# Kernel tuning notes

Measured on AMD Instinct MI355X. Metric: run time of the kernel, lower is better.

## Reference

```python
import jax, jax.numpy as jnp
import numpy as np

EPS_ATTN = 1e-6
EPS_LN = 1e-5


def _layer_norm(x, g, b):
    m = jnp.mean(x, axis=-1, keepdims=True)
    v = jnp.mean((x - m) ** 2, axis=-1, keepdims=True)
    return (x - m) * jax.lax.rsqrt(v + EPS_LN) * g + b


def _linear_attention(q, k, v):
    # q,k,v: [N, L/S, H, D]; elu feature map (+1 keeps values positive)
    q = jax.nn.elu(q) + 1.0
    k = jax.nn.elu(k) + 1.0
    s_len = v.shape[1]
    v = v / s_len
    kv = jnp.einsum('nshd,nshv->nhdv', k, v)            # [N,H,D,D]
    z = 1.0 / (jnp.einsum('nlhd,nhd->nlh', q, k.sum(axis=1)) + EPS_ATTN)
    out = jnp.einsum('nlhd,nhdv->nlhv', q, kv) * z[..., None] * s_len
    return out


def setup_inputs() -> dict:
    key = jax.random.key(0)
    ks = jax.random.split(key, 8)
    N, L, S, H, D = 4, 4096, 4096, 8, 64
    sc = 0.05
    return {
        'x': jax.random.normal(ks[0], (N, L, H, D), jnp.float32),
        'source': jax.random.normal(ks[1], (N, S, H, D), jnp.float32),
        'wq': jax.random.normal(ks[2], (D, D), jnp.float32) * sc,
        'wk': jax.random.normal(ks[3], (D, D), jnp.float32) * sc,
        'wv': jax.random.normal(ks[4], (D, D), jnp.float32) * sc,
        'wmerge': jax.random.normal(ks[5], (D, D), jnp.float32) * sc,
        'w1': jax.random.normal(ks[6], (2 * D, 2 * D), jnp.float32) * sc,
        'w2': jax.random.normal(ks[7], (D, 2 * D), jnp.float32) * sc,
        'g1': jnp.ones((D,), jnp.float32),
        'b1': jnp.zeros((D,), jnp.float32),
        'g2': jnp.ones((D,), jnp.float32),
        'b2': jnp.zeros((D,), jnp.float32),
    }


def reference(x, source, wq, wk, wv, wmerge, w1, w2, g1, b1, g2, b2):
    # projections (torch Linear: y = x @ W.T), applied on last dim D=d_model
    q = jnp.einsum('nlhd,ed->nlhe', x, wq)
    k = jnp.einsum('nshd,ed->nshe', source, wk)
    v = jnp.einsum('nshd,ed->nshe', source, wv)
    message = _linear_attention(q, k, v)                # [N,L,H,D]
    message = jnp.einsum('nlhd,ed->nlhe', message, wmerge)
    message = _layer_norm(message, g1, b1)
    h = jnp.concatenate([x, message], axis=-1)          # [N,L,H,2D]
    h = jax.nn.relu(jnp.einsum('nlhd,ed->nlhe', h, w1))
    h = jnp.einsum('nlhd,ed->nlhe', h, w2)              # [N,L,H,D]
    h = _layer_norm(h, g2, b2)
    return x + h
```

## Files before the change

### kernel.cpp

```cpp
#include <hip/hip_runtime.h>
#include <cstdint>

#define NB 4
#define LL 4096
#define SS 4096
#define HH 8
#define DD 64
#define NHC (NB*HH)

typedef unsigned short ushort_t;
typedef __bf16 bf16x8 __attribute__((ext_vector_type(8)));
typedef float f32x4 __attribute__((ext_vector_type(4)));
typedef unsigned short u16x8 __attribute__((ext_vector_type(8)));
typedef unsigned short u16x4 __attribute__((ext_vector_type(4)));

__device__ __forceinline__ float bf2f(unsigned short u) {
    union { unsigned int i; float f; } v; v.i = ((unsigned int)u) << 16; return v.f;
}
__device__ __forceinline__ unsigned short f2bf(float f) {
    union { float ff; unsigned int i; } v; v.ff = f;
    unsigned int x = v.i;
    x += 0x7fffu + ((x >> 16) & 1u);
    return (unsigned short)(x >> 16);
}
__device__ __forceinline__ bool input_is_bf16(const void* g1) {
    return ((const unsigned short*)g1)[0] == 0x3F80u;
}

template<bool BF16>
__device__ __forceinline__ float ldgf(const void* p, size_t i) {
    if constexpr (BF16) return bf2f(((const unsigned short*)p)[i]);
    else                return ((const float*)p)[i];
}
template<bool BF16>
__device__ __forceinline__ u16x8 ld8(const void* p, size_t i) {
    if constexpr (BF16) {
        return *reinterpret_cast<const u16x8*>((const unsigned short*)p + i);
    } else {
        const float* f = (const float*)p + i;
        u16x8 o;
        #pragma unroll
        for (int j = 0; j < 8; ++j) o[j] = f2bf(f[j]);
        return o;
    }
}
__device__ __forceinline__ bf16x8 ldsA(const ushort_t* p) {
    return *reinterpret_cast<const bf16x8*>(p);
}
#define MFMA16(a,b,c) __builtin_amdgcn_mfma_f32_16x16x32_bf16(a,b,c,0,0,0)

template<bool BF16, int LC>
__device__ __forceinline__ void stage_w(const void* g, size_t goff, ushort_t* dst,
                                        int rows, int dstride, int tid) {
    int total8 = (rows << LC) >> 3;
    for (int i8 = tid; i8 < total8; i8 += 256) {
        int i = i8 << 3;
        int r = i >> LC, c = i & ((1 << LC) - 1);
        *reinterpret_cast<u16x8*>(dst + r * dstride + c) = ld8<BF16>(g, goff + i);
    }
}

__device__ __forceinline__ void red16(float v[4]) {
    #pragma unroll
    for (int m = 1; m < 16; m <<= 1) {
        #pragma unroll
        for (int r = 0; r < 4; ++r) v[r] += __shfl_xor(v[r], m);
    }
}

template<bool BF16>
__device__ void kv_body(const void* __restrict__ src, const void* __restrict__ wk,
                        const void* __restrict__ wv, float* __restrict__ kvg,
                        float* __restrict__ ksumg,
                        ushort_t* S, ushort_t* KT, ushort_t* VT)
{
    const int tid = threadIdx.x;
    const int lane = tid & 63, w = tid >> 6;
    const int lg = lane >> 4, l15 = lane & 15;
    const int bid = blockIdx.x;
    const int nh = bid >> 5, ch = bid & 31;
    const int n = nh >> 3, h = nh & 7;
    const int s0 = ch * 128;
    const f32x4 z4 = {0.f, 0.f, 0.f, 0.f};

    stage_w<BF16, 6>(wk, 0, KT, 64, 136, tid);
    stage_w<BF16, 6>(wv, 0, VT, 64, 136, tid);
    for (int i = tid; i < 128 * 8; i += 256) {
        int r = i >> 3, c8 = (i & 7) << 3;
        size_t gb = ((size_t)((size_t)n * SS + (s0 + r)) * HH + h) * DD + c8;
        *reinterpret_cast<u16x8*>(S + r * 72 + c8) = ld8<BF16>(src, gb);
    }
    __syncthreads();

    bf16x8 wkf[2][4], wvf[2][4];
    #pragma unroll
    for (int ks = 0; ks < 2; ++ks)
        #pragma unroll
        for (int nt = 0; nt < 4; ++nt) {
            wkf[ks][nt] = ldsA(KT + (nt * 16 + l15) * 136 + ks * 32 + lg * 8);
            wvf[ks][nt] = ldsA(VT + (nt * 16 + l15) * 136 + ks * 32 + lg * 8);
        }
    __syncthreads();

    float ksp[4] = {0.f, 0.f, 0.f, 0.f};
    #pragma unroll
    for (int mtt = 0; mtt < 2; ++mtt) {
        const int rowA = w * 32 + mtt * 16;
        bf16x8 af[2];
        #pragma unroll
        for (int ks = 0; ks < 2; ++ks)
            af[ks] = ldsA(S + (rowA + l15) * 72 + ks * 32 + lg * 8);
        f32x4 ka[4], va[4];
        #pragma unroll
        for (int nt = 0; nt < 4; ++nt) { ka[nt] = z4; va[nt] = z4; }
        #pragma unroll
        for (int ks = 0; ks < 2; ++ks)
            #pragma unroll
            for (int nt = 0; nt < 4; ++nt) {
                ka[nt] = MFMA16(af[ks], wkf[ks][nt], ka[nt]);
                va[nt] = MFMA16(af[ks], wvf[ks][nt], va[nt]);
            }
        #pragma unroll
        for (int nt = 0; nt < 4; ++nt) {
            u16x4 kp, vp;
            #pragma unroll
            for (int r = 0; r < 4; ++r) {
                float kvl = ka[nt][r];
                kvl = kvl > 0.f ? kvl + 1.f : __expf(kvl);
                ksp[nt] += kvl;
                kp[r] = f2bf(kvl);
                vp[r] = f2bf(va[nt][r]);
            }
            const int dcol = nt * 16 + l15;
            *reinterpret_cast<u16x4*>(KT + dcol * 136 + rowA + lg * 4) = kp;
            *reinterpret_cast<u16x4*>(VT + dcol * 136 + rowA + lg * 4) = vp;
        }
    }
    __syncthreads();

    f32x4 kvacc[4];
    #pragma unroll
    for (int nt = 0; nt < 4; ++nt) kvacc[nt] = z4;
    #pragma unroll
    for (int ks = 0; ks < 4; ++ks) {
        bf16x8 akv = ldsA(KT + (w * 16 + l15) * 136 + ks * 32 + lg * 8);
        #pragma unroll
        for (int nt = 0; nt < 4; ++nt) {
            bf16x8 bkv = ldsA(VT + (nt * 16 + l15) * 136 + ks * 32 + lg * 8);
            kvacc[nt] = MFMA16(akv, bkv, kvacc[nt]);
        }
    }

    float* kvo = kvg + (size_t)nh * DD * DD;
    #pragma unroll
    for (int nt = 0; nt < 4; ++nt)
        #pragma unroll
        for (int r = 0; r < 4; ++r)
            atomicAdd(&kvo[(w * 16 + lg * 4 + r) * DD + nt * 16 + l15], kvacc[nt][r]);
    #pragma unroll
    for (int m = 16; m < 64; m <<= 1)
        #pragma unroll
        for (int nt = 0; nt < 4; ++nt) ksp[nt] += __shfl_xor(ksp[nt], m);
    if (lane < 16) {
        #pragma unroll
        for (int nt = 0; nt < 4; ++nt)
            atomicAdd(&ksumg[nh * DD + nt * 16 + lane], ksp[nt]);
    }
}

__global__ __launch_bounds__(256, 3) void kv_kernel(
    const void* __restrict__ src, const void* __restrict__ wk, const void* __restrict__ wv,
    const void* __restrict__ g1, float* __restrict__ kvg, float* __restrict__ ksumg)
{
    __shared__ ushort_t S[128 * 72];
    __shared__ ushort_t KT[64 * 136];
    __shared__ ushort_t VT[64 * 136];
    if (input_is_bf16(g1)) kv_body<true >(src, wk, wv, kvg, ksumg, S, KT, VT);
    else                   kv_body<false>(src, wk, wv, kvg, ksumg, S, KT, VT);
}

template<bool BF16>
__device__ void main_body(const void* __restrict__ x,
                          const void* __restrict__ wq, const void* __restrict__ wm,
                          const void* __restrict__ w1, const void* __restrict__ w2,
                          const void* __restrict__ g1, const void* __restrict__ b1,
                          const void* __restrict__ g2, const void* __restrict__ b2,
                          const float* __restrict__ kvg, const float* __restrict__ ksumg,
                          void* __restrict__ outp,
                          ushort_t* w1s, ushort_t* kvs, ushort_t* B0, ushort_t* B1,
                          ushort_t* B2)
{
    const int tid = threadIdx.x;
    const int lane = tid & 63, w = tid >> 6;
    const int lg = lane >> 4, l15 = lane & 15;
    const int bid = blockIdx.x;
    const int nh = bid >> 4, ch = bid & 15;
    const int n = nh >> 3, h = nh & 7;
    const int rowA = w * 16;
    const f32x4 z4 = {0.f, 0.f, 0.f, 0.f};

    auto ldx = [&](int t, u16x8 xv[2]) {
        #pragma unroll
        for (int p = 0; p < 2; ++p) {
            int r16 = p * 8 + (lane >> 3), c8 = (lane & 7) << 3;
            size_t gb = ((size_t)((size_t)n * LL + (ch * 256 + t * 64 + rowA + r16)) * HH + h) * DD + c8;
            xv[p] = ld8<BF16>(x, gb);
        }
    };

    u16x8 xv[2];
    ldx(0, xv);

    stage_w<BF16, 6>(wq, 0, B0, 64, 72, tid);
    stage_w<BF16, 6>(wm, 0, B1, 64, 72, tid);
    stage_w<BF16, 7>(w2, 0, w1s, 64, 136, tid);
    for (int i = tid; i < 4096; i += 256) {
        int d = i >> 6, e = i & 63;
        B2[d * 72 + e] = f2bf(kvg[(size_t)nh * 4096 + i]);
    }
    __syncthreads();

    bf16x8 wqf[2][4], w2f[4][4];
    #pragma unroll
    for (int ks = 0; ks < 2; ++ks)
        #pragma unroll
        for (int nt = 0; nt < 4; ++nt)
            wqf[ks][nt] = ldsA(B0 + (nt * 16 + l15) * 72 + ks * 32 + lg * 8);
    #pragma unroll
    for (int ks = 0; ks < 4; ++ks)
        #pragma unroll
        for (int nt = 0; nt < 4; ++nt)
            w2f[ks][nt] = ldsA(w1s + (nt * 16 + l15) * 136 + ks * 32 + lg * 8);
    {
        bf16x8 akv[2];
        #pragma unroll
        for (int ks = 0; ks < 2; ++ks)
            akv[ks] = ldsA(B2 + (w * 16 + l15) * 72 + ks * 32 + lg * 8);
        f32x4 km[4];
        #pragma unroll
        for (int nt = 0; nt < 4; ++nt) km[nt] = z4;
        #pragma unroll
        for (int ks = 0; ks < 2; ++ks)
            #pragma unroll
            for (int nt = 0; nt < 4; ++nt) {
                bf16x8 bwm = ldsA(B1 + (nt * 16 + l15) * 72 + ks * 32 + lg * 8);
                km[nt] = MFMA16(akv[ks], bwm, km[nt]);
            }
        #pragma unroll
        for (int nt = 0; nt < 4; ++nt)
            #pragma unroll
            for (int r = 0; r < 4; ++r)
                kvs[(nt * 16 + l15) * 72 + w * 16 + lg * 4 + r] = f2bf(km[nt][r]);
    }
    __syncthreads();

    stage_w<BF16, 7>(w1, 0, w1s, 128, 136, tid);
    bf16x8 kvmf[2][4];
    #pragma unroll
    for (int ks = 0; ks < 2; ++ks)
        #pragma unroll
        for (int nt = 0; nt < 4; ++nt)
            kvmf[ks][nt] = ldsA(kvs + (nt * 16 + l15) * 72 + ks * 32 + lg * 8);
    float g1r[4], b1r[4], g2r[4], b2r[4], ksr[4];
    #pragma unroll
    for (int nt = 0; nt < 4; ++nt) {
        int c = nt * 16 + l15;
        g1r[nt] = ldgf<BF16>(g1, c); b1r[nt] = ldgf<BF16>(b1, c);
        g2r[nt] = ldgf<BF16>(g2, c); b2r[nt] = ldgf<BF16>(b2, c);
        ksr[nt] = ksumg[nh * 64 + c];
    }
    __syncthreads();

    for (int t = 0; t < 4; ++t) {
        const int l0 = ch * 256 + t * 64;

        #pragma unroll
        for (int p = 0; p < 2; ++p) {
            int r16 = p * 8 + (lane >> 3), c8 = (lane & 7) << 3;
            *reinterpret_cast<u16x8*>(B0 + (rowA + r16) * 72 + c8) = xv[p];
        }
        u16x8 xn[2];
        if (t < 3) ldx(t + 1, xn);

        bf16x8 af[2];
        #pragma unroll
        for (int ks = 0; ks < 2; ++ks)
            af[ks] = ldsA(B0 + (rowA + l15) * 72 + ks * 32 + lg * 8);
        f32x4 qa[4];
        #pragma unroll
        for (int nt = 0; nt < 4; ++nt) qa[nt] = z4;
        __builtin_amdgcn_s_setprio(1);
        #pragma unroll
        for (int ks = 0; ks < 2; ++ks)
            #pragma unroll
            for (int nt = 0; nt < 4; ++nt)
                qa[nt] = MFMA16(af[ks], wqf[ks][nt], qa[nt]);
        __builtin_amdgcn_s_setprio(0);
        float zp[4] = {0.f, 0.f, 0.f, 0.f};
        #pragma unroll
        for (int nt = 0; nt < 4; ++nt)
            #pragma unroll
            for (int r = 0; r < 4; ++r) {
                float v = qa[nt][r];
                v = v > 0.f ? v + 1.f : __expf(v);
                zp[r] += v * ksr[nt];
                B1[(rowA + lg * 4 + r) * 72 + nt * 16 + l15] = f2bf(v);
            }
        red16(zp);
        float zr[4];
        #pragma unroll
        for (int r = 0; r < 4; ++r) zr[r] = 1.f / (zp[r] + 1e-6f);

        #pragma unroll
        for (int ks = 0; ks < 2; ++ks)
            af[ks] = ldsA(B1 + (rowA + l15) * 72 + ks * 32 + lg * 8);
        f32x4 ma[4];
        #pragma unroll
        for (int nt = 0; nt < 4; ++nt) ma[nt] = z4;
        __builtin_amdgcn_s_setprio(1);
        #pragma unroll
        for (int ks = 0; ks < 2; ++ks)
            #pragma unroll
            for (int nt = 0; nt < 4; ++nt)
                ma[nt] = MFMA16(af[ks], kvmf[ks][nt], ma[nt]);
        __builtin_amdgcn_s_setprio(0);
        #pragma unroll
        for (int nt = 0; nt < 4; ++nt)
            #pragma unroll
            for (int r = 0; r < 4; ++r) ma[nt][r] *= zr[r];

        float s1[4] = {0.f,0.f,0.f,0.f}, s2[4] = {0.f,0.f,0.f,0.f};
        #pragma unroll
        for (int nt = 0; nt < 4; ++nt)
            #pragma unroll
            for (int r = 0; r < 4; ++r) {
                float v = ma[nt][r]; s1[r] += v; s2[r] += v * v;
            }
        red16(s1); red16(s2);
        #pragma unroll
        for (int r = 0; r < 4; ++r) {
            float mu = s1[r] * 0.015625f;
            float var = s2[r] * 0.015625f - mu * mu;
            s1[r] = mu; s2[r] = rsqrtf(var + 1e-5f);
        }
        #pragma unroll
        for (int nt = 0; nt < 4; ++nt)
            #pragma unroll
            for (int r = 0; r < 4; ++r)
                B1[(rowA + lg * 4 + r) * 72 + nt * 16 + l15] =
                    f2bf((ma[nt][r] - s1[r]) * s2[r] * g1r[nt] + b1r[nt]);

        f32x4 ha[4];
        #pragma unroll
        for (int nt = 0; nt < 4; ++nt) ha[nt] = z4;
        #pragma unroll
        for (int half = 0; half < 2; ++half) {
            f32x4 ta[4];
            #pragma unroll
            for (int nt = 0; nt < 4; ++nt) ta[nt] = z4;
            __builtin_amdgcn_s_setprio(1);
            #pragma unroll
            for (int ks = 0; ks < 4; ++ks) {
                const ushort_t* bp = (ks < 2) ? B0 : B1;
                bf16x8 a1 = ldsA(bp + (rowA + l15) * 72 + (ks & 1) * 32 + lg * 8);
                #pragma unroll
                for (int nt = 0; nt < 4; ++nt) {
                    bf16x8 bw = ldsA(w1s + (half * 64 + nt * 16 + l15) * 136 + ks * 32 + lg * 8);
                    ta[nt] = MFMA16(a1, bw, ta[nt]);
                }
            }
            __builtin_amdgcn_s_setprio(0);
            #pragma unroll
            for (int nt = 0; nt < 4; ++nt)
                #pragma unroll
                for (int r = 0; r < 4; ++r)
                    B2[(rowA + lg * 4 + r) * 72 + nt * 16 + l15] =
                        f2bf(fmaxf(ta[nt][r], 0.f));
            __builtin_amdgcn_s_setprio(1);
            #pragma unroll
            for (int k2 = 0; k2 < 2; ++k2) {
                bf16x8 a2 = ldsA(B2 + (rowA + l15) * 72 + k2 * 32 + lg * 8);
                #pragma unroll
                for (int nt = 0; nt < 4; ++nt)
                    ha[nt] = MFMA16(a2, w2f[half * 2 + k2][nt], ha[nt]);
            }
            __builtin_amdgcn_s_setprio(0);
        }

        float t1[4] = {0.f,0.f,0.f,0.f}, t2[4] = {0.f,0.f,0.f,0.f};
        #pragma unroll
        for (int nt = 0; nt < 4; ++nt)
            #pragma unroll
            for (int r = 0; r < 4; ++r) {
                float v = ha[nt][r]; t1[r] += v; t2[r] += v * v;
            }
        red16(t1); red16(t2);
        #pragma unroll
        for (int r = 0; r < 4; ++r) {
            float mu = t1[r] * 0.015625f;
            float var = t2[r] * 0.015625f - mu * mu;
            t1[r] = mu; t2[r] = rsqrtf(var + 1e-5f);
        }
        #pragma unroll
        for (int nt = 0; nt < 4; ++nt)
            #pragma unroll
            for (int r = 0; r < 4; ++r) {
                float xv2 = bf2f(B0[(rowA + lg * 4 + r) * 72 + nt * 16 + l15]);
                float ov = xv2 + (ha[nt][r] - t1[r]) * t2[r] * g2r[nt] + b2r[nt];
                B1[(rowA + lg * 4 + r) * 72 + nt * 16 + l15] = f2bf(ov);
            }

        #pragma unroll
        for (int p = 0; p < 2; ++p) {
            int r16 = p * 8 + (lane >> 3), c8 = (lane & 7) << 3;
            size_t gb = ((size_t)((size_t)n * LL + (l0 + rowA + r16)) * HH + h) * DD + c8;
            u16x8 v = *reinterpret_cast<const u16x8*>(B1 + (rowA + r16) * 72 + c8);
            if constexpr (BF16) {
                *reinterpret_cast<u16x8*>((unsigned short*)outp + gb) = v;
            } else {
                float* fo = (float*)outp + gb;
                #pragma unroll
                for (int j = 0; j < 8; ++j) fo[j] = bf2f(v[j]);
            }
        }

        if (t < 3) { xv[0] = xn[0]; xv[1] = xn[1]; }
    }
}

__global__ __launch_bounds__(256, 2) void main_kernel(
    const void* __restrict__ x,
    const void* __restrict__ wq, const void* __restrict__ wm,
    const void* __restrict__ w1, const void* __restrict__ w2,
    const void* __restrict__ g1, const void* __restrict__ b1,
    const void* __restrict__ g2, const void* __restrict__ b2,
    const float* __restrict__ kvg, const float* __restrict__ ksumg,
    void* __restrict__ outp)
{
    __shared__ ushort_t w1s[128 * 136];
    __shared__ ushort_t kvs[64 * 72];
    __shared__ ushort_t B0[64 * 72];
    __shared__ ushort_t B1[64 * 72];
    __shared__ ushort_t B2[64 * 72];
    if (input_is_bf16(g1))
        main_body<true >(x, wq, wm, w1, w2, g1, b1, g2, b2, kvg, ksumg, outp,
                         w1s, kvs, B0, B1, B2);
    else
        main_body<false>(x, wq, wm, w1, w2, g1, b1, g2, b2, kvg, ksumg, outp,
                         w1s, kvs, B0, B1, B2);
}

extern "C" void kernel_launch(void* const* d_in, const int* in_sizes, int n_in,
                              void* d_out, int out_size, void* d_ws, size_t ws_size,
                              hipStream_t stream) {
    const void* x   = d_in[0];
    const void* src = d_in[1];
    const void* wq  = d_in[2];
    const void* wk  = d_in[3];
    const void* wv  = d_in[4];
    const void* wm  = d_in[5];
    const void* w1  = d_in[6];
    const void* w2  = d_in[7];
    const void* g1  = d_in[8];
    const void* b1  = d_in[9];
    const void* g2  = d_in[10];
    const void* b2  = d_in[11];

    float* kvg   = (float*)d_ws;
    float* ksumg = kvg + (size_t)NHC * DD * DD;

    hipMemsetAsync(d_ws, 0, ((size_t)NHC * DD * DD + NHC * DD) * sizeof(float), stream);
    kv_kernel<<<NHC * 32, 256, 0, stream>>>(src, wk, wv, g1, kvg, ksumg);
    main_kernel<<<NHC * 16, 256, 0, stream>>>(x, wq, wm, w1, w2, g1, b1, g2, b2,
                                              kvg, ksumg, d_out);
}
```

Baseline: 171.0 us.

## Restructure main kernel: XOR-swizzled LDS, stream w1 from global, more blocks

Replaces padded LDS strides with XOR-swizzled layouts and stops staging w1 in LDS, loading its fragments straight from global/L2 per 32-column chunk instead. w2 fragments are now read from LDS on each use rather than held in registers. Together these shrink LDS and register use so three blocks fit per CU. The grid doubles so each block handles 128 rows instead of 256. It also switches f2bf to the native bf16 conversion. The trade-offs are extra global traffic for w1 on every tile, plus more per-block setup (staging weights and the kv·wmerge product) repeated across twice as many blocks.

```diff
diff --git a/kernel.cpp b/kernel.cpp
--- a/kernel.cpp
+++ b/kernel.cpp
@@ -18,10 +18,7 @@
     union { unsigned int i; float f; } v; v.i = ((unsigned int)u) << 16; return v.f;
 }
 __device__ __forceinline__ unsigned short f2bf(float f) {
-    union { float ff; unsigned int i; } v; v.ff = f;
-    unsigned int x = v.i;
-    x += 0x7fffu + ((x >> 16) & 1u);
-    return (unsigned short)(x >> 16);
+    union { __bf16 b; unsigned short u; } v; v.b = (__bf16)f; return v.u;
 }
 __device__ __forceinline__ bool input_is_bf16(const void* g1) {
     return ((const unsigned short*)g1)[0] == 0x3F80u;
@@ -48,6 +45,9 @@
     return *reinterpret_cast<const bf16x8*>(p);
 }
 #define MFMA16(a,b,c) __builtin_amdgcn_mfma_f32_16x16x32_bf16(a,b,c,0,0,0)
+
+__device__ __forceinline__ int sw64(int r, int c)  { return (r << 6) + (c ^ ((r & 7) << 3)); }
+__device__ __forceinline__ int sw128(int r, int c) { return (r << 7) + (c ^ ((r & 7) << 3)); }
 
 template<bool BF16, int LC>
 __device__ __forceinline__ void stage_w(const void* g, size_t goff, ushort_t* dst,
@@ -57,6 +57,28 @@
         int i = i8 << 3;
         int r = i >> LC, c = i & ((1 << LC) - 1);
         *reinterpret_cast<u16x8*>(dst + r * dstride + c) = ld8<BF16>(g, goff + i);
+    }
+}
+template<bool BF16, int LC>
+__device__ __forceinline__ void stage_sw(const void* g, ushort_t* dst, int rows, int tid) {
+    int total8 = (rows << LC) >> 3;
+    for (int i8 = tid; i8 < total8; i8 += 256) {
+        int i = i8 << 3;
+        int r = i >> LC, c = i & ((1 << LC) - 1);
+        int off = (LC == 6) ? sw64(r, c) : sw128(r, c);
+        *reinterpret_cast<u16x8*>(dst + off) = ld8<BF16>(g, i);
+    }
+}
+template<bool BF16>
+__device__ __forceinline__ bf16x8 ldw1(const void* w1, int row, int col) {
+    if constexpr (BF16) {
+        return *reinterpret_cast<const bf16x8*>((const unsigned short*)w1 + row * 128 + col);
+    } else {
+        const float* f = (const float*)w1 + row * 128 + col;
+        bf16x8 o;
+        #pragma unroll
+        for (int j = 0; j < 8; ++j) o[j] = (__bf16)f[j];
+        return o;
     }
 }
 
@@ -187,14 +209,14 @@
                           const void* __restrict__ g2, const void* __restrict__ b2,
                           const float* __restrict__ kvg, const float* __restrict__ ksumg,
                           void* __restrict__ outp,
-                          ushort_t* w1s, ushort_t* kvs, ushort_t* B0, ushort_t* B1,
+                          ushort_t* W2S, ushort_t* KVS, ushort_t* B0, ushort_t* B1,
                           ushort_t* B2)
 {
     const int tid = threadIdx.x;
     const int lane = tid & 63, w = tid >> 6;
     const int lg = lane >> 4, l15 = lane & 15;
     const int bid = blockIdx.x;
-    const int nh = bid >> 4, ch = bid & 15;
+    const int nh = bid >> 5, ch = bid & 31;
     const int n = nh >> 3, h = nh & 7;
     const int rowA = w * 16;
     const f32x4 z4 = {0.f, 0.f, 0.f, 0.f};
@@ -203,7 +225,7 @@
         #pragma unroll
         for (int p = 0; p < 2; ++p) {
             int r16 = p * 8 + (lane >> 3), c8 = (lane & 7) << 3;
-            size_t gb = ((size_t)((size_t)n * LL + (ch * 256 + t * 64 + rowA + r16)) * HH + h) * DD + c8;
+            size_t gb = ((size_t)((size_t)n * LL + (ch * 128 + t * 64 + rowA + r16)) * HH + h) * DD + c8;
             xv[p] = ld8<BF16>(x, gb);
         }
     };
@@ -211,56 +233,51 @@
     u16x8 xv[2];
     ldx(0, xv);
 
-    stage_w<BF16, 6>(wq, 0, B0, 64, 72, tid);
-    stage_w<BF16, 6>(wm, 0, B1, 64, 72, tid);
-    stage_w<BF16, 7>(w2, 0, w1s, 64, 136, tid);
+    stage_sw<BF16, 6>(wq, B0, 64, tid);
+    stage_sw<BF16, 6>(wm, B1, 64, tid);
+    stage_sw<BF16, 7>(w2, W2S, 64, tid);
     for (int i = tid; i < 4096; i += 256) {
         int d = i >> 6, e = i & 63;
-        B2[d * 72 + e] = f2bf(kvg[(size_t)nh * 4096 + i]);
-    }
-    __syncthreads();
-
-    bf16x8 wqf[2][4], w2f[4][4];
+        KVS[sw64(d, e)] = f2bf(kvg[(size_t)nh * 4096 + i]);
+    }
+    __syncthreads();
+
+    bf16x8 wqf[2][4];
     #pragma unroll
     for (int ks = 0; ks < 2; ++ks)
         #pragma unroll
         for (int nt = 0; nt < 4; ++nt)
-            wqf[ks][nt] = ldsA(B0 + (nt * 16 + l15) * 72 + ks * 32 + lg * 8);
-    #pragma unroll
-    for (int ks = 0; ks < 4; ++ks)
-        #pragma unroll
-        for (int nt = 0; nt < 4; ++nt)
-            w2f[ks][nt] = ldsA(w1s + (nt * 16 + l15) * 136 + ks * 32 + lg * 8);
-    {
-        bf16x8 akv[2];
-        #pragma unroll
-        for (int ks = 0; ks < 2; ++ks)
-            akv[ks] = ldsA(B2 + (w * 16 + l15) * 72 + ks * 32 + lg * 8);
-        f32x4 km[4];
-        #pragma unroll
-        for (int nt = 0; nt < 4; ++nt) km[nt] = z4;
-        #pragma unroll
-        for (int ks = 0; ks < 2; ++ks)
-            #pragma unroll
-            for (int nt = 0; nt < 4; ++nt) {
-                bf16x8 bwm = ldsA(B1 + (nt * 16 + l15) * 72 + ks * 32 + lg * 8);
-                km[nt] = MFMA16(akv[ks], bwm, km[nt]);
-            }
-        #pragma unroll
-        for (int nt = 0; nt < 4; ++nt)
-            #pragma unroll
-            for (int r = 0; r < 4; ++r)
-                kvs[(nt * 16 + l15) * 72 + w * 16 + lg * 4 + r] = f2bf(km[nt][r]);
-    }
-    __syncthreads();
-
-    stage_w<BF16, 7>(w1, 0, w1s, 128, 136, tid);
+            wqf[ks][nt] = ldsA(B0 + sw64(nt * 16 + l15, ks * 32 + lg * 8));
+    bf16x8 akv[2];
+    #pragma unroll
+    for (int ks = 0; ks < 2; ++ks)
+        akv[ks] = ldsA(KVS + sw64(w * 16 + l15, ks * 32 + lg * 8));
+    f32x4 km[4];
+    #pragma unroll
+    for (int nt = 0; nt < 4; ++nt) km[nt] = z4;
+    #pragma unroll
+    for (int ks = 0; ks < 2; ++ks)
+        #pragma unroll
+        for (int nt = 0; nt < 4; ++nt) {
+            bf16x8 bwm = ldsA(B1 + sw64(nt * 16 + l15, ks * 32 + lg * 8));
+            km[nt] = MFMA16(akv[ks], bwm, km[nt]);
+        }
+    __syncthreads();
+    #pragma unroll
+    for (int nt = 0; nt < 4; ++nt) {
+        u16x4 kp;
+        #pragma unroll
+        for (int r = 0; r < 4; ++r) kp[r] = f2bf(km[nt][r]);
+        *reinterpret_cast<u16x4*>(KVS + sw64(nt * 16 + l15, w * 16 + lg * 4)) = kp;
+    }
+    __syncthreads();
+
     bf16x8 kvmf[2][4];
     #pragma unroll
     for (int ks = 0; ks < 2; ++ks)
         #pragma unroll
         for (int nt = 0; nt < 4; ++nt)
-            kvmf[ks][nt] = ldsA(kvs + (nt * 16 + l15) * 72 + ks * 32 + lg * 8);
+            kvmf[ks][nt] = ldsA(KVS + sw64(nt * 16 + l15, ks * 32 + lg * 8));
     float g1r[4], b1r[4], g2r[4], b2r[4], ksr[4];
     #pragma unroll
     for (int nt = 0; nt < 4; ++nt) {
@@ -269,23 +286,22 @@
         g2r[nt] = ldgf<BF16>(g2, c); b2r[nt] = ldgf<BF16>(b2, c);
         ksr[nt] = ksumg[nh * 64 + c];
     }
-    __syncthreads();
-
-    for (int t = 0; t < 4; ++t) {
-        const int l0 = ch * 256 + t * 64;
+
+    for (int t = 0; t < 2; ++t) {
+        const int l0 = ch * 128 + t * 64;
 
         #pragma unroll
         for (int p = 0; p < 2; ++p) {
             int r16 = p * 8 + (lane >> 3), c8 = (lane & 7) << 3;
-            *reinterpret_cast<u16x8*>(B0 + (rowA + r16) * 72 + c8) = xv[p];
+            *reinterpret_cast<u16x8*>(B0 + sw64(rowA + r16, c8)) = xv[p];
         }
         u16x8 xn[2];
-        if (t < 3) ldx(t + 1, xn);
+        if (t == 0) ldx(1, xn);
 
         bf16x8 af[2];
         #pragma unroll
         for (int ks = 0; ks < 2; ++ks)
-            af[ks] = ldsA(B0 + (rowA + l15) * 72 + ks * 32 + lg * 8);
+            af[ks] = ldsA(B0 + sw64(rowA + l15, ks * 32 + lg * 8));
         f32x4 qa[4];
         #pragma unroll
         for (int nt = 0; nt < 4; ++nt) qa[nt] = z4;
@@ -304,7 +320,7 @@
                 float v = qa[nt][r];
                 v = v > 0.f ? v + 1.f : __expf(v);
                 zp[r] += v * ksr[nt];
-                B1[(rowA + lg * 4 + r) * 72 + nt * 16 + l15] = f2bf(v);
+                B1[sw64(rowA + lg * 4 + r, nt * 16 + l15)] = f2bf(v);
             }
         red16(zp);
         float zr[4];
@@ -313,7 +329,7 @@
 
         #pragma unroll
         for (int ks = 0; ks < 2; ++ks)
-            af[ks] = ldsA(B1 + (rowA + l15) * 72 + ks * 32 + lg * 8);
+            af[ks] = ldsA(B1 + sw64(rowA + l15, ks * 32 + lg * 8));
         f32x4 ma[4];
         #pragma unroll
         for (int nt = 0; nt < 4; ++nt) ma[nt] = z4;
@@ -347,42 +363,44 @@
         for (int nt = 0; nt < 4; ++nt)
             #pragma unroll
             for (int r = 0; r < 4; ++r)
-                B1[(rowA + lg * 4 + r) * 72 + nt * 16 + l15] =
+                B1[sw64(rowA + lg * 4 + r, nt * 16 + l15)] =
                     f2bf((ma[nt][r] - s1[r]) * s2[r] * g1r[nt] + b1r[nt]);
 
         f32x4 ha[4];
         #pragma unroll
         for (int nt = 0; nt < 4; ++nt) ha[nt] = z4;
         #pragma unroll
-        for (int half = 0; half < 2; ++half) {
-            f32x4 ta[4];
-            #pragma unroll
-            for (int nt = 0; nt < 4; ++nt) ta[nt] = z4;
+        for (int q = 0; q < 4; ++q) {
+            bf16x8 bw[4][2];
+            #pragma unroll
+            for (int ks = 0; ks < 4; ++ks)
+                #pragma unroll
+                for (int nt = 0; nt < 2; ++nt)
+                    bw[ks][nt] = ldw1<BF16>(w1, q * 32 + nt * 16 + l15, ks * 32 + lg * 8);
+            f32x4 ta[2];
+            ta[0] = z4; ta[1] = z4;
             __builtin_amdgcn_s_setprio(1);
             #pragma unroll
             for (int ks = 0; ks < 4; ++ks) {
                 const ushort_t* bp = (ks < 2) ? B0 : B1;
-                bf16x8 a1 = ldsA(bp + (rowA + l15) * 72 + (ks & 1) * 32 + lg * 8);
+                bf16x8 a1 = ldsA(bp + sw64(rowA + l15, (ks & 1) * 32 + lg * 8));
                 #pragma unroll
-                for (int nt = 0; nt < 4; ++nt) {
-                    bf16x8 bw = ldsA(w1s + (half * 64 + nt * 16 + l15) * 136 + ks * 32 + lg * 8);
-                    ta[nt] = MFMA16(a1, bw, ta[nt]);
-                }
+                for (int nt = 0; nt < 2; ++nt)
+                    ta[nt] = MFMA16(a1, bw[ks][nt], ta[nt]);
             }
             __builtin_amdgcn_s_setprio(0);
             #pragma unroll
-            for (int nt = 0; nt < 4; ++nt)
+            for (int nt = 0; nt < 2; ++nt)
                 #pragma unroll
                 for (int r = 0; r < 4; ++r)
-                    B2[(rowA + lg * 4 + r) * 72 + nt * 16 + l15] =
+                    B2[(rowA + lg * 4 + r) * 40 + nt * 16 + l15] =
                         f2bf(fmaxf(ta[nt][r], 0.f));
+            bf16x8 a2 = ldsA(B2 + (rowA + l15) * 40 + lg * 8);
             __builtin_amdgcn_s_setprio(1);
             #pragma unroll
-            for (int k2 = 0; k2 < 2; ++k2) {
-                bf16x8 a2 = ldsA(B2 + (rowA + l15) * 72 + k2 * 32 + lg * 8);
-                #pragma unroll
-                for (int nt = 0; nt < 4; ++nt)
-                    ha[nt] = MFMA16(a2, w2f[half * 2 + k2][nt], ha[nt]);
+            for (int nt = 0; nt < 4; ++nt) {
+                bf16x8 w2b = ldsA(W2S + sw128(nt * 16 + l15, q * 32 + lg * 8));
+                ha[nt] = MFMA16(a2, w2b, ha[nt]);
             }
             __builtin_amdgcn_s_setprio(0);
         }
@@ -405,16 +423,16 @@
         for (int nt = 0; nt < 4; ++nt)
             #pragma unroll
             for (int r = 0; r < 4; ++r) {
-                float xv2 = bf2f(B0[(rowA + lg * 4 + r) * 72 + nt * 16 + l15]);
+                float xv2 = bf2f(B0[sw64(rowA + lg * 4 + r, nt * 16 + l15)]);
                 float ov = xv2 + (ha[nt][r] - t1[r]) * t2[r] * g2r[nt] + b2r[nt];
-                B1[(rowA + lg * 4 + r) * 72 + nt * 16 + l15] = f2bf(ov);
+                B1[sw64(rowA + lg * 4 + r, nt * 16 + l15)] = f2bf(ov);
             }
 
         #pragma unroll
         for (int p = 0; p < 2; ++p) {
             int r16 = p * 8 + (lane >> 3), c8 = (lane & 7) << 3;
             size_t gb = ((size_t)((size_t)n * LL + (l0 + rowA + r16)) * HH + h) * DD + c8;
-            u16x8 v = *reinterpret_cast<const u16x8*>(B1 + (rowA + r16) * 72 + c8);
+            u16x8 v = *reinterpret_cast<const u16x8*>(B1 + sw64(rowA + r16, c8));
             if constexpr (BF16) {
                 *reinterpret_cast<u16x8*>((unsigned short*)outp + gb) = v;
             } else {
@@ -424,11 +442,11 @@
             }
         }
 
-        if (t < 3) { xv[0] = xn[0]; xv[1] = xn[1]; }
-    }
-}
-
-__global__ __launch_bounds__(256, 2) void main_kernel(
+        if (t == 0) { xv[0] = xn[0]; xv[1] = xn[1]; }
+    }
+}
+
+__global__ __launch_bounds__(256, 3) void main_kernel(
     const void* __restrict__ x,
     const void* __restrict__ wq, const void* __restrict__ wm,
     const void* __restrict__ w1, const void* __restrict__ w2,
@@ -437,17 +455,17 @@
     const float* __restrict__ kvg, const float* __restrict__ ksumg,
     void* __restrict__ outp)
 {
-    __shared__ ushort_t w1s[128 * 136];
-    __shared__ ushort_t kvs[64 * 72];
-    __shared__ ushort_t B0[64 * 72];
-    __shared__ ushort_t B1[64 * 72];
-    __shared__ ushort_t B2[64 * 72];
+    __shared__ ushort_t W2S[64 * 128];
+    __shared__ ushort_t KVS[64 * 64];
+    __shared__ ushort_t B0[64 * 64];
+    __shared__ ushort_t B1[64 * 64];
+    __shared__ ushort_t B2[64 * 40];
     if (input_is_bf16(g1))
         main_body<true >(x, wq, wm, w1, w2, g1, b1, g2, b2, kvg, ksumg, outp,
-                         w1s, kvs, B0, B1, B2);
+                         W2S, KVS, B0, B1, B2);
     else
         main_body<false>(x, wq, wm, w1, w2, g1, b1, g2, b2, kvg, ksumg, outp,
-                         w1s, kvs, B0, B1, B2);
+                         W2S, KVS, B0, B1, B2);
 }
 
 extern "C" void kernel_launch(void* const* d_in, const int* in_sizes, int n_in,
@@ -471,6 +489,6 @@
 
     hipMemsetAsync(d_ws, 0, ((size_t)NHC * DD * DD + NHC * DD) * sizeof(float), stream);
     kv_kernel<<<NHC * 32, 256, 0, stream>>>(src, wk, wv, g1, kvg, ksumg);
-    main_kernel<<<NHC * 16, 256, 0, stream>>>(x, wq, wm, w1, w2, g1, b1, g2, b2,
+    main_kernel<<<NHC * 32, 256, 0, stream>>>(x, wq, wm, w1, w2, g1, b1, g2, b2,
                                               kvg, ksumg, d_out);
 }
```

Result: slower. 321.0 us (+87.7%).
